# Optimization experiments

Measured on AMD Instinct MI355X. Metric: run time of the kernel, lower is better.

Reference implementation:

```python
import jax, jax.numpy as jnp
import numpy as np

B, D, R = 8192, 4096, 64
REG_W, REG_C = 0.01, 0.05


def setup_inputs() -> dict:
    key = jax.random.key(0)
    ks = jax.random.split(key, 7)
    return {
        "X": jax.random.normal(ks[0], (B, D), dtype=jnp.float32),
        "U1": jax.random.normal(ks[1], (1, D, R), dtype=jnp.float32),
        "U2": jax.random.normal(ks[2], (2, D, R), dtype=jnp.float32),
        "U3": jax.random.normal(ks[3], (3, D, R), dtype=jnp.float32),
        "C": jax.random.normal(ks[4], (3,), dtype=jnp.float32),
        "beta": jax.random.normal(ks[5], (1,), dtype=jnp.float32),
        "C_sin": jax.random.normal(ks[6], (1,), dtype=jnp.float32),
    }


def reference(X, U1, U2, U3, C, beta, C_sin):
    # term_j(x) = sum_r prod_{i<=j} <x, U_j[i, :, r]>
    result = jnp.broadcast_to(beta[0], (X.shape[0],))
    reg_loss_w = jnp.float32(0.0)
    for j, U in enumerate((U1, U2, U3)):
        dots = jnp.einsum("bd,odr->obr", X, U)      # [order, B, R]
        term = jnp.prod(dots, axis=0).sum(axis=1)   # [B]
        result = result + C[j] * term
        reg_loss_w = reg_loss_w + REG_W * (jnp.abs(U).sum() / U.size)
    sine_term = C_sin[0] * jnp.sin(X).sum(axis=1)
    result = result + sine_term
    reg_loss_c = REG_C * (jnp.abs(C).sum() + jnp.abs(C_sin).sum())
    total_reg = reg_loss_w + reg_loss_c
    return result, total_reg
```

## Files before the change

kernel.cpp:

```cpp
#include <hip/hip_runtime.h>
#include <hip/hip_bf16.h>

typedef float f32x4 __attribute__((ext_vector_type(4)));
typedef short s16x8 __attribute__((ext_vector_type(8)));

#define D_DIM 4096
#define NT 24
#define NSLAB 128
#define BM 32
#define DSTRIDE 388
#define SIN_OFF 49664
#define POOL_BYTES 49920

__device__ __forceinline__ unsigned short f2bf(float f) {
    unsigned u = __float_as_uint(f);
    u += 0x7fffu + ((u >> 16) & 1u);
    return (unsigned short)(u >> 16);
}

__global__ __launch_bounds__(64) void reg_init_kernel(const float* __restrict__ C,
                                                      const float* __restrict__ Csin,
                                                      float* __restrict__ reg_out) {
    if (threadIdx.x == 0)
        reg_out[0] = 0.05f * (fabsf(C[0]) + fabsf(C[1]) + fabsf(C[2]) + fabsf(Csin[0]));
}

__global__ __launch_bounds__(64) void build_w_kernel(const float* __restrict__ U1,
                                                     const float* __restrict__ U2,
                                                     const float* __restrict__ U3,
                                                     unsigned short* __restrict__ W,
                                                     float* __restrict__ reg_out) {
    const int ks = blockIdx.x / NT;
    const int ct = blockIdx.x % NT;
    const int l  = threadIdx.x;
    const int n  = ct * 16 + (l & 15);
    const int kb = ks * 32 + ((l >> 4) << 3);

    const float* src;
    float scale;
    if (n < 64)       { src = U1 + n;                  scale = 0.01f / 262144.f; }
    else if (n < 128) { src = U2 + (n - 64);           scale = 0.01f / 524288.f; }
    else if (n < 192) { src = U2 + 262144 + (n - 128); scale = 0.01f / 524288.f; }
    else if (n < 256) { src = U3 + (n - 192);          scale = 0.01f / 786432.f; }
    else if (n < 320) { src = U3 + 262144 + (n - 256); scale = 0.01f / 786432.f; }
    else              { src = U3 + 524288 + (n - 320); scale = 0.01f / 786432.f; }

    unsigned short h[8];
    float sabs = 0.f;
#pragma unroll
    for (int j = 0; j < 8; ++j) {
        float u = src[(size_t)(kb + j) * 64];
        sabs += fabsf(u);
        h[j] = f2bf(u);
    }
    uint4 pk;
    pk.x = (unsigned)h[0] | ((unsigned)h[1] << 16);
    pk.y = (unsigned)h[2] | ((unsigned)h[3] << 16);
    pk.z = (unsigned)h[4] | ((unsigned)h[5] << 16);
    pk.w = (unsigned)h[6] | ((unsigned)h[7] << 16);
    *(uint4*)(W + ((size_t)blockIdx.x * 64 + l) * 8) = pk;

    sabs *= scale;
#pragma unroll
    for (int off = 32; off >= 1; off >>= 1)
        sabs += __shfl_xor(sabs, off, 64);
    if (l == 0) atomicAdd(reg_out, sabs);
}

__global__ __launch_bounds__(1024) void poly_main_kernel(const float* __restrict__ X,
                                                         const unsigned short* __restrict__ W,
                                                         const float* __restrict__ C,
                                                         const float* __restrict__ beta,
                                                         const float* __restrict__ Csin,
                                                         float* __restrict__ out) {
    __shared__ __align__(16) char pool[POOL_BYTES];

    const int t    = threadIdx.x;
    const int lane = t & 63;
    const int wv   = t >> 6;
    const int kg   = wv >> 3;
    const int cg   = wv & 7;
    const int ct0  = cg * 3;
    const int row0 = blockIdx.x * BM;

    const bool isStage = ((t >> 8) & 1) == 0;
    const int p    = t >> 9;
    const int srow = (t >> 3) & 31;
    const int k4   = (t & 7) << 2;
    const float* xp = X + (size_t)(row0 + srow) * D_DIM + k4;
    const int awfrag = (srow >> 4) * 1024
                     + (((((k4 >> 3) & 3) << 4) | (srow & 15)) * 16) + ((k4 & 7) << 1);

    const s16x8* __restrict__ Wf = (const s16x8*)W;

    f32x4 acc00{}, acc01{}, acc02{}, acc10{}, acc11{}, acc12{};
    float sinacc = 0.f;
    f32x4 xw{}, xa{}, xb{};

    if (isStage) {
        f32x4 x0 = *(const f32x4*)(xp + (size_t)p * 32);
        sinacc += __sinf(x0.x) + __sinf(x0.y) + __sinf(x0.z) + __sinf(x0.w);
        short4 h;
        h.x = (short)f2bf(x0.x); h.y = (short)f2bf(x0.y);
        h.z = (short)f2bf(x0.z); h.w = (short)f2bf(x0.w);
        *(short4*)(pool + p * 2048 + awfrag) = h;
        xw = *(const f32x4*)(xp + (size_t)(2 + p) * 32);
        xa = *(const f32x4*)(xp + (size_t)(4 + p) * 32);
        xb = *(const f32x4*)(xp + (size_t)(6 + p) * 32);
    }
    s16x8 bA0 = Wf[((size_t)kg * NT + ct0 + 0) * 64 + lane];
    s16x8 bA1 = Wf[((size_t)kg * NT + ct0 + 1) * 64 + lane];
    s16x8 bA2 = Wf[((size_t)kg * NT + ct0 + 2) * 64 + lane];
    s16x8 bB0 = Wf[((size_t)(2 + kg) * NT + ct0 + 0) * 64 + lane];
    s16x8 bB1 = Wf[((size_t)(2 + kg) * NT + ct0 + 1) * 64 + lane];
    s16x8 bB2 = Wf[((size_t)(2 + kg) * NT + ct0 + 2) * 64 + lane];
    s16x8 bC0{}, bC1{}, bC2{};
    asm volatile("s_waitcnt lgkmcnt(0)" ::: "memory");
    __builtin_amdgcn_s_barrier();
    __builtin_amdgcn_sched_barrier(0);

#define BODY(d_, U0, U1, U2, P0, P1, P2, XW)                                    \
    {                                                                           \
        const int d__ = (d_);                                                   \
        if (isStage) {                                                          \
            const int sw_ = 2 * d__ + 2 + p;                                    \
            if (sw_ < NSLAB) {                                                  \
                sinacc += __sinf(XW.x) + __sinf(XW.y)                           \
                        + __sinf(XW.z) + __sinf(XW.w);                          \
                short4 h_;                                                      \
                h_.x = (short)f2bf(XW.x); h_.y = (short)f2bf(XW.y);             \
                h_.z = (short)f2bf(XW.z); h_.w = (short)f2bf(XW.w);             \
                *(short4*)(pool + (sw_ & 3) * 2048 + awfrag) = h_;              \
            }                                                                   \
            int sl_ = 2 * d__ + 8 + p; if (sl_ > NSLAB - 1) sl_ = NSLAB - 1;    \
            XW = *(const f32x4*)(xp + (size_t)sl_ * 32);                        \
        }                                                                       \
        int sp_ = 2 * d__ + 4 + kg; if (sp_ > NSLAB - 1) sp_ = NSLAB - 1;       \
        P0 = Wf[((size_t)sp_ * NT + ct0 + 0) * 64 + lane];                      \
        P1 = Wf[((size_t)sp_ * NT + ct0 + 1) * 64 + lane];                      \
        P2 = Wf[((size_t)sp_ * NT + ct0 + 2) * 64 + lane];                      \
        const int ab_ = ((2 * d__ + kg) & 3) * 2048;                            \
        s16x8 af0_ = *(const s16x8*)(pool + ab_ + lane * 16);                   \
        s16x8 af1_ = *(const s16x8*)(pool + ab_ + 1024 + lane * 16);            \
        asm volatile("s_waitcnt lgkmcnt(0)" ::: "memory");                      \
        __builtin_amdgcn_sched_barrier(0);                                      \
        __builtin_amdgcn_s_setprio(1);                                          \
        acc00 = __builtin_amdgcn_mfma_f32_16x16x32_bf16(af0_, U0, acc00, 0, 0, 0); \
        acc01 = __builtin_amdgcn_mfma_f32_16x16x32_bf16(af0_, U1, acc01, 0, 0, 0); \
        acc02 = __builtin_amdgcn_mfma_f32_16x16x32_bf16(af0_, U2, acc02, 0, 0, 0); \
        acc10 = __builtin_amdgcn_mfma_f32_16x16x32_bf16(af1_, U0, acc10, 0, 0, 0); \
        acc11 = __builtin_amdgcn_mfma_f32_16x16x32_bf16(af1_, U1, acc11, 0, 0, 0); \
        acc12 = __builtin_amdgcn_mfma_f32_16x16x32_bf16(af1_, U2, acc12, 0, 0, 0); \
        __builtin_amdgcn_s_setprio(0);                                          \
        __builtin_amdgcn_s_barrier();                                           \
        __builtin_amdgcn_sched_barrier(0);                                      \
    }

    for (int e = 0; e < 21; ++e) {
        BODY(3 * e,     bA0, bA1, bA2, bC0, bC1, bC2, xw);
        BODY(3 * e + 1, bB0, bB1, bB2, bA0, bA1, bA2, xa);
        BODY(3 * e + 2, bC0, bC1, bC2, bB0, bB1, bB2, xb);
    }
    BODY(63, bA0, bA1, bA2, bC0, bC1, bC2, xw);
#undef BODY

    float* Dm = (float*)pool;
    float* sinpart = (float*)(pool + SIN_OFF);
    const f32x4 accA[2][3] = {{acc00, acc01, acc02}, {acc10, acc11, acc12}};
    const int lr4 = (lane >> 4) << 2;
    const int lc  = lane & 15;

    if (kg == 0) {
#pragma unroll
        for (int f = 0; f < 2; ++f)
#pragma unroll
            for (int c = 0; c < 3; ++c) {
                const int col = (ct0 + c) * 16 + lc;
#pragma unroll
                for (int i = 0; i < 4; ++i)
                    Dm[(f * 16 + lr4 + i) * DSTRIDE + col] = accA[f][c][i];
            }
    }
    if (isStage) {
        sinacc += __shfl_xor(sinacc, 1);
        sinacc += __shfl_xor(sinacc, 2);
        sinacc += __shfl_xor(sinacc, 4);
        if ((t & 7) == 0) sinpart[p * 32 + srow] = sinacc;
    }
    __syncthreads();
    if (kg == 1) {
#pragma unroll
        for (int f = 0; f < 2; ++f)
#pragma unroll
            for (int c = 0; c < 3; ++c) {
                const int col = (ct0 + c) * 16 + lc;
#pragma unroll
                for (int i = 0; i < 4; ++i)
                    Dm[(f * 16 + lr4 + i) * DSTRIDE + col] += accA[f][c][i];
            }
    }
    __syncthreads();

    if (t < 512) {
        const int crow = t >> 4;
        const int cc   = t & 15;
        float t1 = 0.f, t2 = 0.f, t3 = 0.f;
#pragma unroll
        for (int rr = 0; rr < 64; rr += 16) {
            const int r = rr + cc;
            t1 += Dm[crow * DSTRIDE + r];
            t2 += Dm[crow * DSTRIDE + 64 + r]  * Dm[crow * DSTRIDE + 128 + r];
            t3 += Dm[crow * DSTRIDE + 192 + r] * Dm[crow * DSTRIDE + 256 + r]
                                               * Dm[crow * DSTRIDE + 320 + r];
        }
#pragma unroll
        for (int off = 1; off < 16; off <<= 1) {
            t1 += __shfl_xor(t1, off, 16);
            t2 += __shfl_xor(t2, off, 16);
            t3 += __shfl_xor(t3, off, 16);
        }
        if (cc == 0)
            out[row0 + crow] = beta[0] + C[0] * t1 + C[1] * t2 + C[2] * t3
                             + Csin[0] * (sinpart[crow] + sinpart[32 + crow]);
    }
}

extern "C" void kernel_launch(void* const* d_in, const int* in_sizes, int n_in,
                              void* d_out, int out_size, void* d_ws, size_t ws_size,
                              hipStream_t stream) {
    const float* X   = (const float*)d_in[0];
    const float* U1  = (const float*)d_in[1];
    const float* U2  = (const float*)d_in[2];
    const float* U3  = (const float*)d_in[3];
    const float* Cc  = (const float*)d_in[4];
    const float* bet = (const float*)d_in[5];
    const float* Cs  = (const float*)d_in[6];
    float* out = (float*)d_out;
    unsigned short* W = (unsigned short*)d_ws;

    reg_init_kernel<<<1, 64, 0, stream>>>(Cc, Cs, out + 8192);
    build_w_kernel<<<128 * NT, 64, 0, stream>>>(U1, U2, U3, W, out + 8192);
    poly_main_kernel<<<256, 1024, 0, stream>>>(X, W, Cc, bet, Cs, out);
}
```

Baseline: 93.43 us.

## Split K across two blocks with 64-row tiles and add combine kernel

Each block now handles 64 rows but only half of the D dimension, so W fragments are reused across twice as many rows and every thread stages X, not just half of them. Partial dot products are written to a global workspace together with per-half sine sums, and a new combine kernel adds the two halves and evaluates the polynomial terms. The goal is to halve W traffic per row and raise MFMA work per barrier. In exchange it adds a kernel launch and extra global traffic for the partials (about 25 MB written and read back), and it doubles accumulator register use.

```diff
diff --git a/kernel.cpp b/kernel.cpp
--- a/kernel.cpp
+++ b/kernel.cpp
@@ -6,11 +6,12 @@
 
 #define D_DIM 4096
 #define NT 24
-#define NSLAB 128
-#define BM 32
-#define DSTRIDE 388
-#define SIN_OFF 49664
-#define POOL_BYTES 49920
+#define NSLAB_H 64
+#define BM 64
+#define DSTRIDE 392
+#define POOL_BYTES (64 * DSTRIDE * 4)
+#define PART_OFF (4u << 20)
+#define SINW_OFF (28u << 20)
 
 __device__ __forceinline__ unsigned short f2bf(float f) {
     unsigned u = __float_as_uint(f);
@@ -69,10 +70,8 @@
 
 __global__ __launch_bounds__(1024) void poly_main_kernel(const float* __restrict__ X,
                                                          const unsigned short* __restrict__ W,
-                                                         const float* __restrict__ C,
-                                                         const float* __restrict__ beta,
-                                                         const float* __restrict__ Csin,
-                                                         float* __restrict__ out) {
+                                                         float* __restrict__ part,
+                                                         float* __restrict__ sinws) {
     __shared__ __align__(16) char pool[POOL_BYTES];
 
     const int t    = threadIdx.x;
@@ -81,40 +80,42 @@
     const int kg   = wv >> 3;
     const int cg   = wv & 7;
     const int ct0  = cg * 3;
-    const int row0 = blockIdx.x * BM;
-
-    const bool isStage = ((t >> 8) & 1) == 0;
+    const int rb   = blockIdx.x >> 1;
+    const int kh   = blockIdx.x & 1;
+    const int row0 = rb * BM;
+
     const int p    = t >> 9;
-    const int srow = (t >> 3) & 31;
+    const int srow = (t >> 3) & 63;
     const int k4   = (t & 7) << 2;
-    const float* xp = X + (size_t)(row0 + srow) * D_DIM + k4;
+    const float* xp = X + (size_t)(row0 + srow) * D_DIM + kh * 2048 + k4;
     const int awfrag = (srow >> 4) * 1024
                      + (((((k4 >> 3) & 3) << 4) | (srow & 15)) * 16) + ((k4 & 7) << 1);
 
-    const s16x8* __restrict__ Wf = (const s16x8*)W;
-
-    f32x4 acc00{}, acc01{}, acc02{}, acc10{}, acc11{}, acc12{};
+    const s16x8* __restrict__ Wh = (const s16x8*)W + (size_t)kh * NSLAB_H * NT * 64;
+
+    f32x4 acc[4][3];
+#pragma unroll
+    for (int r = 0; r < 4; ++r)
+#pragma unroll
+        for (int c = 0; c < 3; ++c) acc[r][c] = (f32x4){0.f, 0.f, 0.f, 0.f};
     float sinacc = 0.f;
     f32x4 xw{}, xa{}, xb{};
 
-    if (isStage) {
+    {
         f32x4 x0 = *(const f32x4*)(xp + (size_t)p * 32);
         sinacc += __sinf(x0.x) + __sinf(x0.y) + __sinf(x0.z) + __sinf(x0.w);
         short4 h;
         h.x = (short)f2bf(x0.x); h.y = (short)f2bf(x0.y);
         h.z = (short)f2bf(x0.z); h.w = (short)f2bf(x0.w);
-        *(short4*)(pool + p * 2048 + awfrag) = h;
+        *(short4*)(pool + p * 4096 + awfrag) = h;
         xw = *(const f32x4*)(xp + (size_t)(2 + p) * 32);
         xa = *(const f32x4*)(xp + (size_t)(4 + p) * 32);
         xb = *(const f32x4*)(xp + (size_t)(6 + p) * 32);
     }
-    s16x8 bA0 = Wf[((size_t)kg * NT + ct0 + 0) * 64 + lane];
-    s16x8 bA1 = Wf[((size_t)kg * NT + ct0 + 1) * 64 + lane];
-    s16x8 bA2 = Wf[((size_t)kg * NT + ct0 + 2) * 64 + lane];
-    s16x8 bB0 = Wf[((size_t)(2 + kg) * NT + ct0 + 0) * 64 + lane];
-    s16x8 bB1 = Wf[((size_t)(2 + kg) * NT + ct0 + 1) * 64 + lane];
-    s16x8 bB2 = Wf[((size_t)(2 + kg) * NT + ct0 + 2) * 64 + lane];
-    s16x8 bC0{}, bC1{}, bC2{};
+    s16x8 bA0 = Wh[((size_t)kg * NT + ct0 + 0) * 64 + lane];
+    s16x8 bA1 = Wh[((size_t)kg * NT + ct0 + 1) * 64 + lane];
+    s16x8 bA2 = Wh[((size_t)kg * NT + ct0 + 2) * 64 + lane];
+    s16x8 bB0{}, bB1{}, bB2{};
     asm volatile("s_waitcnt lgkmcnt(0)" ::: "memory");
     __builtin_amdgcn_s_barrier();
     __builtin_amdgcn_sched_barrier(0);
@@ -122,106 +123,140 @@
 #define BODY(d_, U0, U1, U2, P0, P1, P2, XW)                                    \
     {                                                                           \
         const int d__ = (d_);                                                   \
-        if (isStage) {                                                          \
-            const int sw_ = 2 * d__ + 2 + p;                                    \
-            if (sw_ < NSLAB) {                                                  \
-                sinacc += __sinf(XW.x) + __sinf(XW.y)                           \
-                        + __sinf(XW.z) + __sinf(XW.w);                          \
-                short4 h_;                                                      \
-                h_.x = (short)f2bf(XW.x); h_.y = (short)f2bf(XW.y);             \
-                h_.z = (short)f2bf(XW.z); h_.w = (short)f2bf(XW.w);             \
-                *(short4*)(pool + (sw_ & 3) * 2048 + awfrag) = h_;              \
-            }                                                                   \
-            int sl_ = 2 * d__ + 8 + p; if (sl_ > NSLAB - 1) sl_ = NSLAB - 1;    \
-            XW = *(const f32x4*)(xp + (size_t)sl_ * 32);                        \
+        const int sw_ = 2 * d__ + 2 + p;                                        \
+        if (sw_ < NSLAB_H) {                                                    \
+            sinacc += __sinf(XW.x) + __sinf(XW.y)                               \
+                    + __sinf(XW.z) + __sinf(XW.w);                              \
+            short4 h_;                                                          \
+            h_.x = (short)f2bf(XW.x); h_.y = (short)f2bf(XW.y);                 \
+            h_.z = (short)f2bf(XW.z); h_.w = (short)f2bf(XW.w);                 \
+            *(short4*)(pool + (sw_ & 3) * 4096 + awfrag) = h_;                  \
         }                                                                       \
-        int sp_ = 2 * d__ + 4 + kg; if (sp_ > NSLAB - 1) sp_ = NSLAB - 1;       \
-        P0 = Wf[((size_t)sp_ * NT + ct0 + 0) * 64 + lane];                      \
-        P1 = Wf[((size_t)sp_ * NT + ct0 + 1) * 64 + lane];                      \
-        P2 = Wf[((size_t)sp_ * NT + ct0 + 2) * 64 + lane];                      \
-        const int ab_ = ((2 * d__ + kg) & 3) * 2048;                            \
-        s16x8 af0_ = *(const s16x8*)(pool + ab_ + lane * 16);                   \
-        s16x8 af1_ = *(const s16x8*)(pool + ab_ + 1024 + lane * 16);            \
+        int sl_ = 2 * d__ + 8 + p; if (sl_ > NSLAB_H - 1) sl_ = NSLAB_H - 1;    \
+        XW = *(const f32x4*)(xp + (size_t)sl_ * 32);                            \
+        int sp_ = 2 * d__ + 2 + kg; if (sp_ > NSLAB_H - 1) sp_ = NSLAB_H - 1;   \
+        P0 = Wh[((size_t)sp_ * NT + ct0 + 0) * 64 + lane];                      \
+        P1 = Wh[((size_t)sp_ * NT + ct0 + 1) * 64 + lane];                      \
+        P2 = Wh[((size_t)sp_ * NT + ct0 + 2) * 64 + lane];                      \
+        const int ab_ = ((2 * d__ + kg) & 3) * 4096;                            \
+        s16x8 af0_ = *(const s16x8*)(pool + ab_ + 0 * 1024 + lane * 16);        \
+        s16x8 af1_ = *(const s16x8*)(pool + ab_ + 1 * 1024 + lane * 16);        \
+        s16x8 af2_ = *(const s16x8*)(pool + ab_ + 2 * 1024 + lane * 16);        \
+        s16x8 af3_ = *(const s16x8*)(pool + ab_ + 3 * 1024 + lane * 16);        \
         asm volatile("s_waitcnt lgkmcnt(0)" ::: "memory");                      \
         __builtin_amdgcn_sched_barrier(0);                                      \
         __builtin_amdgcn_s_setprio(1);                                          \
-        acc00 = __builtin_amdgcn_mfma_f32_16x16x32_bf16(af0_, U0, acc00, 0, 0, 0); \
-        acc01 = __builtin_amdgcn_mfma_f32_16x16x32_bf16(af0_, U1, acc01, 0, 0, 0); \
-        acc02 = __builtin_amdgcn_mfma_f32_16x16x32_bf16(af0_, U2, acc02, 0, 0, 0); \
-        acc10 = __builtin_amdgcn_mfma_f32_16x16x32_bf16(af1_, U0, acc10, 0, 0, 0); \
-        acc11 = __builtin_amdgcn_mfma_f32_16x16x32_bf16(af1_, U1, acc11, 0, 0, 0); \
-        acc12 = __builtin_amdgcn_mfma_f32_16x16x32_bf16(af1_, U2, acc12, 0, 0, 0); \
+        acc[0][0] = __builtin_amdgcn_mfma_f32_16x16x32_bf16(af0_, U0, acc[0][0], 0, 0, 0); \
+        acc[0][1] = __builtin_amdgcn_mfma_f32_16x16x32_bf16(af0_, U1, acc[0][1], 0, 0, 0); \
+        acc[0][2] = __builtin_amdgcn_mfma_f32_16x16x32_bf16(af0_, U2, acc[0][2], 0, 0, 0); \
+        acc[1][0] = __builtin_amdgcn_mfma_f32_16x16x32_bf16(af1_, U0, acc[1][0], 0, 0, 0); \
+        acc[1][1] = __builtin_amdgcn_mfma_f32_16x16x32_bf16(af1_, U1, acc[1][1], 0, 0, 0); \
+        acc[1][2] = __builtin_amdgcn_mfma_f32_16x16x32_bf16(af1_, U2, acc[1][2], 0, 0, 0); \
+        acc[2][0] = __builtin_amdgcn_mfma_f32_16x16x32_bf16(af2_, U0, acc[2][0], 0, 0, 0); \
+        acc[2][1] = __builtin_amdgcn_mfma_f32_16x16x32_bf16(af2_, U1, acc[2][1], 0, 0, 0); \
+        acc[2][2] = __builtin_amdgcn_mfma_f32_16x16x32_bf16(af2_, U2, acc[2][2], 0, 0, 0); \
+        acc[3][0] = __builtin_amdgcn_mfma_f32_16x16x32_bf16(af3_, U0, acc[3][0], 0, 0, 0); \
+        acc[3][1] = __builtin_amdgcn_mfma_f32_16x16x32_bf16(af3_, U1, acc[3][1], 0, 0, 0); \
+        acc[3][2] = __builtin_amdgcn_mfma_f32_16x16x32_bf16(af3_, U2, acc[3][2], 0, 0, 0); \
         __builtin_amdgcn_s_setprio(0);                                          \
         __builtin_amdgcn_s_barrier();                                           \
         __builtin_amdgcn_sched_barrier(0);                                      \
     }
 
-    for (int e = 0; e < 21; ++e) {
-        BODY(3 * e,     bA0, bA1, bA2, bC0, bC1, bC2, xw);
-        BODY(3 * e + 1, bB0, bB1, bB2, bA0, bA1, bA2, xa);
-        BODY(3 * e + 2, bC0, bC1, bC2, bB0, bB1, bB2, xb);
-    }
-    BODY(63, bA0, bA1, bA2, bC0, bC1, bC2, xw);
+    for (int e = 0; e < 5; ++e) {
+        const int d0 = 6 * e;
+        BODY(d0 + 0, bA0, bA1, bA2, bB0, bB1, bB2, xw);
+        BODY(d0 + 1, bB0, bB1, bB2, bA0, bA1, bA2, xa);
+        BODY(d0 + 2, bA0, bA1, bA2, bB0, bB1, bB2, xb);
+        BODY(d0 + 3, bB0, bB1, bB2, bA0, bA1, bA2, xw);
+        BODY(d0 + 4, bA0, bA1, bA2, bB0, bB1, bB2, xa);
+        BODY(d0 + 5, bB0, bB1, bB2, bA0, bA1, bA2, xb);
+    }
+    BODY(30, bA0, bA1, bA2, bB0, bB1, bB2, xw);
+    BODY(31, bB0, bB1, bB2, bA0, bA1, bA2, xa);
 #undef BODY
 
     float* Dm = (float*)pool;
-    float* sinpart = (float*)(pool + SIN_OFF);
-    const f32x4 accA[2][3] = {{acc00, acc01, acc02}, {acc10, acc11, acc12}};
     const int lr4 = (lane >> 4) << 2;
     const int lc  = lane & 15;
 
     if (kg == 0) {
 #pragma unroll
-        for (int f = 0; f < 2; ++f)
+        for (int r = 0; r < 4; ++r)
 #pragma unroll
             for (int c = 0; c < 3; ++c) {
                 const int col = (ct0 + c) * 16 + lc;
 #pragma unroll
                 for (int i = 0; i < 4; ++i)
-                    Dm[(f * 16 + lr4 + i) * DSTRIDE + col] = accA[f][c][i];
+                    Dm[(r * 16 + lr4 + i) * DSTRIDE + col] = acc[r][c][i];
             }
-    }
-    if (isStage) {
-        sinacc += __shfl_xor(sinacc, 1);
-        sinacc += __shfl_xor(sinacc, 2);
-        sinacc += __shfl_xor(sinacc, 4);
-        if ((t & 7) == 0) sinpart[p * 32 + srow] = sinacc;
     }
     __syncthreads();
     if (kg == 1) {
 #pragma unroll
-        for (int f = 0; f < 2; ++f)
+        for (int r = 0; r < 4; ++r)
 #pragma unroll
             for (int c = 0; c < 3; ++c) {
                 const int col = (ct0 + c) * 16 + lc;
 #pragma unroll
                 for (int i = 0; i < 4; ++i)
-                    Dm[(f * 16 + lr4 + i) * DSTRIDE + col] += accA[f][c][i];
+                    Dm[(r * 16 + lr4 + i) * DSTRIDE + col] += acc[r][c][i];
             }
     }
+    sinacc += __shfl_xor(sinacc, 1);
+    sinacc += __shfl_xor(sinacc, 2);
+    sinacc += __shfl_xor(sinacc, 4);
+    if ((t & 7) == 0)
+        sinws[(size_t)(kh * 2 + p) * 8192 + row0 + srow] = sinacc;
     __syncthreads();
 
-    if (t < 512) {
-        const int crow = t >> 4;
-        const int cc   = t & 15;
-        float t1 = 0.f, t2 = 0.f, t3 = 0.f;
-#pragma unroll
-        for (int rr = 0; rr < 64; rr += 16) {
-            const int r = rr + cc;
-            t1 += Dm[crow * DSTRIDE + r];
-            t2 += Dm[crow * DSTRIDE + 64 + r]  * Dm[crow * DSTRIDE + 128 + r];
-            t3 += Dm[crow * DSTRIDE + 192 + r] * Dm[crow * DSTRIDE + 256 + r]
-                                               * Dm[crow * DSTRIDE + 320 + r];
-        }
-#pragma unroll
-        for (int off = 1; off < 16; off <<= 1) {
-            t1 += __shfl_xor(t1, off, 16);
-            t2 += __shfl_xor(t2, off, 16);
-            t3 += __shfl_xor(t3, off, 16);
-        }
-        if (cc == 0)
-            out[row0 + crow] = beta[0] + C[0] * t1 + C[1] * t2 + C[2] * t3
-                             + Csin[0] * (sinpart[crow] + sinpart[32 + crow]);
+    float* pb = part + ((size_t)kh * 128 + rb) * (BM * 384);
+    const int prow = t >> 4;
+    const int pc0  = (t & 15) * 24;
+#pragma unroll
+    for (int v = 0; v < 6; ++v)
+        *(f32x4*)(pb + (size_t)prow * 384 + pc0 + v * 4) =
+            *(const f32x4*)(Dm + prow * DSTRIDE + pc0 + v * 4);
+}
+
+__global__ __launch_bounds__(512) void combine_kernel(const float* __restrict__ part,
+                                                      const float* __restrict__ sinws,
+                                                      const float* __restrict__ C,
+                                                      const float* __restrict__ beta,
+                                                      const float* __restrict__ Csin,
+                                                      float* __restrict__ out) {
+    const int t   = threadIdx.x;
+    const int row = blockIdx.x * 32 + (t >> 4);
+    const int cc  = t & 15;
+    const int rb  = row >> 6;
+    const int lr  = row & 63;
+    const float* p0 = part + (size_t)rb * (64 * 384) + (size_t)lr * 384;
+    const float* p1 = p0 + (size_t)128 * (64 * 384);
+
+    float t1 = 0.f, t2 = 0.f, t3 = 0.f;
+#pragma unroll
+    for (int rr = 0; rr < 64; rr += 16) {
+        const int c = rr + cc;
+        const float d1 = p0[c]       + p1[c];
+        const float a2 = p0[64 + c]  + p1[64 + c];
+        const float b2 = p0[128 + c] + p1[128 + c];
+        const float a3 = p0[192 + c] + p1[192 + c];
+        const float b3 = p0[256 + c] + p1[256 + c];
+        const float c3 = p0[320 + c] + p1[320 + c];
+        t1 += d1;
+        t2 += a2 * b2;
+        t3 += a3 * b3 * c3;
+    }
+#pragma unroll
+    for (int off = 1; off < 16; off <<= 1) {
+        t1 += __shfl_xor(t1, off, 16);
+        t2 += __shfl_xor(t2, off, 16);
+        t3 += __shfl_xor(t3, off, 16);
+    }
+    if (cc == 0) {
+        const float s = sinws[row] + sinws[8192 + row]
+                      + sinws[2 * 8192 + row] + sinws[3 * 8192 + row];
+        out[row] = beta[0] + C[0] * t1 + C[1] * t2 + C[2] * t3 + Csin[0] * s;
     }
 }
 
@@ -236,9 +271,13 @@
     const float* bet = (const float*)d_in[5];
     const float* Cs  = (const float*)d_in[6];
     float* out = (float*)d_out;
+
     unsigned short* W = (unsigned short*)d_ws;
+    float* part  = (float*)((char*)d_ws + PART_OFF);
+    float* sinws = (float*)((char*)d_ws + SINW_OFF);
 
     reg_init_kernel<<<1, 64, 0, stream>>>(Cc, Cs, out + 8192);
     build_w_kernel<<<128 * NT, 64, 0, stream>>>(U1, U2, U3, W, out + 8192);
-    poly_main_kernel<<<256, 1024, 0, stream>>>(X, W, Cc, bet, Cs, out);
-}
+    poly_main_kernel<<<256, 1024, 0, stream>>>(X, W, part, sinws);
+    combine_kernel<<<256, 512, 0, stream>>>(part, sinws, Cc, bet, Cs, out);
+}
```

Result: slower. 99.93 us (+7.0%).
